# Performance work log

Hardware: AMD Instinct MI355X
Metric: run time of the kernel (lower is better)

The kernel has to match this reference:

```python
import jax, jax.numpy as jnp
import numpy as np

NUM_HEADS = 16


def setup_inputs() -> dict:
    key = jax.random.key(0)
    k1, k2, k3, k4 = jax.random.split(key, 4)
    B, N, C = 4, 2048, 1024
    x = jax.random.normal(k1, (B, N, C), dtype=jnp.float32)
    # xavier-uniform-ish scaling for stable softmax
    Wqkv = jax.random.normal(k2, (C, 3 * C), dtype=jnp.float32) * (2.0 / (C + 3 * C)) ** 0.5
    Wproj = jax.random.normal(k3, (C, C), dtype=jnp.float32) * (1.0 / C) ** 0.5
    bproj = jnp.zeros((C,), dtype=jnp.float32)
    mask = jax.random.randint(k4, (B, N), 0, 2, dtype=jnp.int32)  # >0 means masked
    return {"x": x, "Wqkv": Wqkv, "Wproj": Wproj, "bproj": bproj, "mask": mask}


def reference(x, Wqkv, Wproj, bproj, mask):
    B, N, C = x.shape
    H = NUM_HEADS
    Dh = C // H
    scale = Dh ** -0.5
    qkv = x @ Wqkv                                   # [B, N, 3C]
    qkv = qkv.reshape(B, N, 3, H, Dh).transpose(2, 0, 3, 1, 4)  # [3, B, H, N, Dh]
    q, k, v = qkv[0], qkv[1], qkv[2]
    att = jnp.einsum('bhqd,bhkd->bhqk', q, k) * scale  # [B, H, N, N]
    att = jnp.where(mask[:, None, None, :] > 0, jnp.float32(-10000000.0), att)
    att = jax.nn.softmax(att, axis=-1)
    out = jnp.einsum('bhqk,bhkd->bhqd', att, v)      # [B, H, N, Dh]
    out = out.transpose(0, 2, 1, 3).reshape(B, N, C)
    return out @ Wproj + bproj
```

## Files before the change

### kernel.cpp

```cpp
#include <hip/hip_runtime.h>
#include <hip/hip_bf16.h>
#include <cstdint>

typedef __bf16 bf16x8 __attribute__((ext_vector_type(8)));
typedef float f32x4 __attribute__((ext_vector_type(4)));
typedef uint4 __attribute__((may_alias)) uint4a;
typedef uint2 __attribute__((may_alias)) uint2a;

typedef __attribute__((address_space(3))) unsigned int   lds_u32;
typedef __attribute__((address_space(1))) const unsigned int gbl_u32;

#define BATCH 4
#define SEQ   2048
#define CDIM  1024
#define NH    16
#define HD    64

#define C1SCALE 0.18033688011112042f

__device__ __forceinline__ unsigned short f2bf(float f) {
    uint32_t u = __builtin_bit_cast(uint32_t, f);
    u += 0x7fffu + ((u >> 16) & 1u);
    return (unsigned short)(u >> 16);
}

#if __has_builtin(__builtin_amdgcn_cvt_pk_bf16_f32)
typedef __bf16 bf16x2 __attribute__((ext_vector_type(2)));
__device__ __forceinline__ uint32_t pk2bf(float a, float b) {
    bf16x2 v = __builtin_amdgcn_cvt_pk_bf16_f32(a, b);
    return __builtin_bit_cast(uint32_t, v);
}
#else
__device__ __forceinline__ uint32_t pk2bf(float a, float b) {
    return (uint32_t)f2bf(a) | ((uint32_t)f2bf(b) << 16);
}
#endif

__device__ __forceinline__ void g2l16(const unsigned short* g, unsigned short* l) {
    __builtin_amdgcn_global_load_lds((gbl_u32*)g, (lds_u32*)l, 16, 0, 0);
}

#define NB_CVT   8192
#define NB_TQKV  768
#define NB_TPROJ 256
#define NB_PREP  (NB_CVT + NB_TQKV + NB_TPROJ + 4)

__global__ __launch_bounds__(256)
void prep_kernel(const float* __restrict__ x,
                 const float* __restrict__ Wqkv,
                 const float* __restrict__ Wproj,
                 const int* __restrict__ mask,
                 unsigned short* __restrict__ xb,
                 unsigned short* __restrict__ Wqkvt,
                 unsigned short* __restrict__ Wprojt,
                 int* __restrict__ ridx, int* __restrict__ cnt) {
    __shared__ float tile[64][65];
    __shared__ int s[256];
    int bid = blockIdx.x, tid = threadIdx.x;

    if (bid < NB_CVT) {
        int i = (bid * 256 + tid) * 4;
        float4 v = *(const float4*)(x + i);
        uint2 o;
        o.x = pk2bf(v.x, v.y);
        o.y = pk2bf(v.z, v.w);
        *(uint2*)(xb + i) = o;
        return;
    }
    if (bid < NB_CVT + NB_TQKV + NB_TPROJ) {
        const float* in;
        unsigned short* out;
        int Cc, bx;
        if (bid < NB_CVT + NB_TQKV) {
            bx = bid - NB_CVT; in = Wqkv; out = Wqkvt; Cc = 3072;
        } else {
            bx = bid - NB_CVT - NB_TQKV; in = Wproj; out = Wprojt; Cc = 1024;
        }
        int nbx = Cc >> 6;
        int c0 = (bx % nbx) * 64, r0 = (bx / nbx) * 64;
        int tx = tid & 63, ty = tid >> 6;
        #pragma unroll
        for (int i = 0; i < 64; i += 4)
            tile[ty + i][tx] = in[(size_t)(r0 + ty + i) * Cc + c0 + tx];
        __syncthreads();
        #pragma unroll
        for (int i = 0; i < 64; i += 4)
            out[(size_t)(c0 + ty + i) * 1024 + r0 + tx] = f2bf(tile[tx][ty + i]);
        return;
    }
    int b = bid - (NB_CVT + NB_TQKV + NB_TPROJ);
    int keep[8], lc = 0;
    #pragma unroll
    for (int u = 0; u < 8; ++u) {
        keep[u] = (mask[b * SEQ + tid * 8 + u] > 0) ? 0 : 1;
        lc += keep[u];
    }
    s[tid] = lc;
    __syncthreads();
    for (int d = 1; d < 256; d <<= 1) {
        int w = (tid >= d) ? s[tid - d] : 0;
        __syncthreads();
        s[tid] += w;
        __syncthreads();
    }
    int pos = s[tid] - lc;
    #pragma unroll
    for (int u = 0; u < 8; ++u) {
        if (keep[u]) ridx[b * SEQ + pos++] = tid * 8 + u;
    }
    int total = s[255];
    for (int i = total + tid; i < SEQ; i += 256)
        ridx[b * SEQ + i] = 0;
    if (tid == 255) cnt[b] = total;
}

#define BK 64

__global__ __launch_bounds__(256, 2)
void gemm_qkv2_kernel(const unsigned short* __restrict__ A,
                      const unsigned short* __restrict__ Bt,
                      const int* __restrict__ ridx,
                      const int* __restrict__ cnt,
                      unsigned short* __restrict__ Q,
                      unsigned short* __restrict__ Kc,
                      unsigned short* __restrict__ Vct) {
    __shared__ __align__(16) unsigned short sA[128 * 64];
    __shared__ __align__(16) unsigned short sB[128 * 64];
    const int Kdim = 1024;
    int tid = threadIdx.x;
    int wave = tid >> 6, lane = tid & 63;
    int wm = (wave >> 1) * 64, wn = (wave & 1) * 64;
    int l15 = lane & 15, quad = lane >> 4;
    int lr = lane >> 3, lc8 = ((lane & 7) ^ lr) * 8;

    const bool qpath = (blockIdx.y < 8);
    int m0, n0, b = 0, kn = 0;
    const unsigned short* aPtr[4];

    if (qpath) {
        m0 = blockIdx.x * 128;
        n0 = blockIdx.y * 128;
        #pragma unroll
        for (int it = 0; it < 4; ++it) {
            int gr = (wave * 4 + it) * 8 + lr;
            aPtr[it] = A + (size_t)(m0 + gr) * Kdim + lc8;
        }
    } else {
        b  = blockIdx.x >> 4;
        m0 = (blockIdx.x & 15) * 128;
        kn = cnt[b];
        if (m0 >= kn) return;
        n0 = 1024 + (blockIdx.y - 8) * 128;
        #pragma unroll
        for (int it = 0; it < 4; ++it) {
            int gr = (wave * 4 + it) * 8 + lr;
            int rid = ridx[b * SEQ + m0 + gr];
            aPtr[it] = A + (size_t)(b * SEQ + rid) * Kdim + lc8;
        }
    }

    f32x4 acc[4][4] = {};

    for (int k0 = 0; k0 < Kdim; k0 += BK) {
        #pragma unroll
        for (int it = 0; it < 4; ++it) {
            int c = wave * 4 + it;
            int gr = c * 8 + lr;
            g2l16(aPtr[it] + k0, &sA[c * 512]);
            g2l16(Bt + (size_t)(n0 + gr) * Kdim + k0 + lc8, &sB[c * 512]);
        }
        __syncthreads();
        #pragma unroll
        for (int kk = 0; kk < BK; kk += 32) {
            bf16x8 af[4], bfr[4];
            #pragma unroll
            for (int i = 0; i < 4; ++i) {
                int r = wm + i * 16 + l15;
                int q = ((kk >> 3) + quad) ^ (r & 7);
                af[i] = __builtin_bit_cast(bf16x8, *(const uint4a*)(&sA[r * 64 + q * 8]));
            }
            #pragma unroll
            for (int j = 0; j < 4; ++j) {
                int r = wn + j * 16 + l15;
                int q = ((kk >> 3) + quad) ^ (r & 7);
                bfr[j] = __builtin_bit_cast(bf16x8, *(const uint4a*)(&sB[r * 64 + q * 8]));
            }
            #pragma unroll
            for (int i = 0; i < 4; ++i)
                #pragma unroll
                for (int j = 0; j < 4; ++j)
                    acc[i][j] = __builtin_amdgcn_mfma_f32_16x16x32_bf16(af[i], bfr[j], acc[i][j], 0, 0, 0);
        }
        __syncthreads();
    }

    if (qpath) {
        #pragma unroll
        for (int i = 0; i < 4; ++i) {
            #pragma unroll
            for (int j = 0; j < 4; ++j) {
                int col = n0 + wn + j * 16 + l15;
                int h = col >> 6;
                int d = col & 63;
                int row0 = m0 + wm + i * 16 + quad * 4;
                int bb = row0 >> 11, n = row0 & 2047;
                size_t bh = (size_t)(bb * NH + h);
                uint32_t p01 = pk2bf(acc[i][j][0] * C1SCALE, acc[i][j][1] * C1SCALE);
                uint32_t p23 = pk2bf(acc[i][j][2] * C1SCALE, acc[i][j][3] * C1SCALE);
                size_t base = (bh * SEQ + n) * HD + d;
                Q[base]          = (unsigned short)p01;
                Q[base + HD]     = (unsigned short)(p01 >> 16);
                Q[base + 2 * HD] = (unsigned short)p23;
                Q[base + 3 * HD] = (unsigned short)(p23 >> 16);
            }
        }
    } else {
        #pragma unroll
        for (int i = 0; i < 4; ++i) {
            #pragma unroll
            for (int j = 0; j < 4; ++j) {
                int c2 = (n0 - 1024) + wn + j * 16 + l15;
                int three = c2 >> 10;
                int h = (c2 >> 6) & 15;
                int d = c2 & 63;
                int pf0 = m0 + wm + i * 16 + quad * 4;
                size_t bh = (size_t)(b * NH + h);
                if (three == 0) {
                    #pragma unroll
                    for (int r = 0; r < 4; ++r) {
                        int pf = pf0 + r;
                        if (pf < kn) Kc[(bh * SEQ + pf) * HD + d] = f2bf(acc[i][j][r]);
                    }
                } else {
                    #pragma unroll
                    for (int r = 0; r < 4; ++r) {
                        int pf = pf0 + r;
                        if (pf < kn) Vct[(bh * HD + d) * SEQ + pf] = f2bf(acc[i][j][r]);
                    }
                }
            }
        }
    }
}

__global__ __launch_bounds__(256, 2)
void gemm_proj_kernel(const unsigned short* __restrict__ A,
                      const unsigned short* __restrict__ Bt,
                      const float* __restrict__ bias,
                      float* __restrict__ Out) {
    __shared__ __align__(16) unsigned short sA[128 * 64];
    __shared__ __align__(16) unsigned short sB[128 * 64];
    const int Kdim = 1024;
    int m0 = blockIdx.x * 128;
    int n0 = blockIdx.y * 128;
    int tid = threadIdx.x;
    int wave = tid >> 6, lane = tid & 63;
    int wm = (wave >> 1) * 64, wn = (wave & 1) * 64;
    int l15 = lane & 15, quad = lane >> 4;
    int lr = lane >> 3, lc8 = ((lane & 7) ^ lr) * 8;

    f32x4 acc[4][4] = {};

    for (int k0 = 0; k0 < Kdim; k0 += BK) {
        #pragma unroll
        for (int it = 0; it < 4; ++it) {
            int c = wave * 4 + it;
            int gr = c * 8 + lr;
            g2l16(A  + (size_t)(m0 + gr) * Kdim + k0 + lc8, &sA[c * 512]);
            g2l16(Bt + (size_t)(n0 + gr) * Kdim + k0 + lc8, &sB[c * 512]);
        }
        __syncthreads();
        #pragma unroll
        for (int kk = 0; kk < BK; kk += 32) {
            bf16x8 af[4], bfr[4];
            #pragma unroll
            for (int i = 0; i < 4; ++i) {
                int r = wm + i * 16 + l15;
                int q = ((kk >> 3) + quad) ^ (r & 7);
                af[i] = __builtin_bit_cast(bf16x8, *(const uint4a*)(&sA[r * 64 + q * 8]));
            }
            #pragma unroll
            for (int j = 0; j < 4; ++j) {
                int r = wn + j * 16 + l15;
                int q = ((kk >> 3) + quad) ^ (r & 7);
                bfr[j] = __builtin_bit_cast(bf16x8, *(const uint4a*)(&sB[r * 64 + q * 8]));
            }
            #pragma unroll
            for (int i = 0; i < 4; ++i)
                #pragma unroll
                for (int j = 0; j < 4; ++j)
                    acc[i][j] = __builtin_amdgcn_mfma_f32_16x16x32_bf16(af[i], bfr[j], acc[i][j], 0, 0, 0);
        }
        __syncthreads();
    }

    #pragma unroll
    for (int i = 0; i < 4; ++i) {
        #pragma unroll
        for (int j = 0; j < 4; ++j) {
            int col = n0 + wn + j * 16 + l15;
            float bv = bias[col];
            #pragma unroll
            for (int r = 0; r < 4; ++r) {
                int row = m0 + wm + i * 16 + quad * 4 + r;
                Out[(size_t)row * CDIM + col] = acc[i][j][r] + bv;
            }
        }
    }
}

#define SPD 72

__global__ __launch_bounds__(256, 4)
void flash_attn_kernel(const unsigned short* __restrict__ Q,
                       const unsigned short* __restrict__ Kg,
                       const unsigned short* __restrict__ Vt,
                       const int* __restrict__ cnt,
                       unsigned short* __restrict__ O) {
    int bh = blockIdx.x;
    int q0 = blockIdx.y * 128;
    int b = bh >> 4, h = bh & 15;
    int tid = threadIdx.x;
    int wave = tid >> 6, lane = tid & 63;
    int l15 = lane & 15, quad = lane >> 4;
    int lr = lane >> 3, lc8 = ((lane & 7) ^ lr) * 8;

    const int kn = cnt[b];

    const size_t head_off = (size_t)bh * SEQ * HD;
    const unsigned short* Qh = Q + head_off;
    const unsigned short* Kh = Kg + head_off;
    const unsigned short* Vh = Vt + head_off;

    __shared__ __align__(16) unsigned short sK [64 * 64];
    __shared__ __align__(16) unsigned short sVt[64 * 64];
    __shared__ __align__(16) unsigned short sP [4][32 * SPD];

    bf16x8 qf[2][2];
    #pragma unroll
    for (int mt = 0; mt < 2; ++mt) {
        const unsigned short* qp = Qh + (size_t)(q0 + wave * 32 + mt * 16 + l15) * HD + quad * 8;
        qf[mt][0] = __builtin_bit_cast(bf16x8, *(const uint4a*)(qp));
        qf[mt][1] = __builtin_bit_cast(bf16x8, *(const uint4a*)(qp + 32));
    }

    bf16x8 ones;
    {
        uint4 ov;
        ov.x = ov.y = ov.z = ov.w = 0x3F803F80u;
        ones = __builtin_bit_cast(bf16x8, ov);
    }

    f32x4 oacc[2][4] = {};
    f32x4 oextra[2] = {};

    for (int k0 = 0; k0 < kn; k0 += 64) {
        #pragma unroll
        for (int it = 0; it < 2; ++it) {
            int c = wave * 2 + it;
            int gr = c * 8 + lr;
            g2l16(Kh + (size_t)(k0 + gr) * HD + lc8, &sK[c * 512]);
            g2l16(Vh + (size_t)gr * SEQ + k0 + lc8, &sVt[c * 512]);
        }
        __syncthreads();

        bool tail = (k0 + 64 > kn);

        f32x4 s[2][4] = {};
        #pragma unroll
        for (int j = 0; j < 4; ++j) {
            int r = j * 16 + l15, sw = r & 7;
            uint4 v0 = *(const uint4a*)(&sK[r * 64 + ((quad ^ sw) * 8)]);
            uint4 v1 = *(const uint4a*)(&sK[r * 64 + (((4 + quad) ^ sw) * 8)]);
            bf16x8 k0f = __builtin_bit_cast(bf16x8, v0);
            bf16x8 k1f = __builtin_bit_cast(bf16x8, v1);
            __builtin_amdgcn_s_setprio(1);
            s[0][j] = __builtin_amdgcn_mfma_f32_16x16x32_bf16(k0f, qf[0][0], s[0][j], 0, 0, 0);
            s[0][j] = __builtin_amdgcn_mfma_f32_16x16x32_bf16(k1f, qf[0][1], s[0][j], 0, 0, 0);
            s[1][j] = __builtin_amdgcn_mfma_f32_16x16x32_bf16(k0f, qf[1][0], s[1][j], 0, 0, 0);
            s[1][j] = __builtin_amdgcn_mfma_f32_16x16x32_bf16(k1f, qf[1][1], s[1][j], 0, 0, 0);
            __builtin_amdgcn_s_setprio(0);
        }

        unsigned short* sp = &sP[wave][0];
        #pragma unroll
        for (int mt = 0; mt < 2; ++mt) {
            int row = mt * 16 + l15;
            #pragma unroll
            for (int j = 0; j < 4; ++j) {
                if (tail) {
                    int kb = k0 + j * 16 + quad * 4;
                    #pragma unroll
                    for (int r = 0; r < 4; ++r)
                        s[mt][j][r] = __builtin_amdgcn_exp2f(s[mt][j][r] + ((kb + r < kn) ? 0.f : -1e30f));
                } else {
                    #pragma unroll
                    for (int r = 0; r < 4; ++r)
                        s[mt][j][r] = __builtin_amdgcn_exp2f(s[mt][j][r]);
                }
                uint2 wv;
                wv.x = pk2bf(s[mt][j][0], s[mt][j][1]);
                wv.y = pk2bf(s[mt][j][2], s[mt][j][3]);
                *(uint2a*)(&sp[row * SPD + j * 16 + quad * 4]) = wv;
            }
        }

        #pragma unroll
        for (int kc = 0; kc < 2; ++kc) {
            uint4 a0 = *(const uint4a*)(&sp[(l15)      * SPD + kc * 32 + quad * 8]);
            uint4 a1 = *(const uint4a*)(&sp[(16 + l15) * SPD + kc * 32 + quad * 8]);
            bf16x8 af0 = __builtin_bit_cast(bf16x8, a0);
            bf16x8 af1 = __builtin_bit_cast(bf16x8, a1);
            __builtin_amdgcn_s_setprio(1);
            #pragma unroll
            for (int jd = 0; jd < 4; ++jd) {
                int r = jd * 16 + l15;
                int q = ((kc * 4 + quad) ^ (r & 7)) * 8;
                uint4 bv = *(const uint4a*)(&sVt[r * 64 + q]);
                bf16x8 vf = __builtin_bit_cast(bf16x8, bv);
                oacc[0][jd] = __builtin_amdgcn_mfma_f32_16x16x32_bf16(af0, vf, oacc[0][jd], 0, 0, 0);
                oacc[1][jd] = __builtin_amdgcn_mfma_f32_16x16x32_bf16(af1, vf, oacc[1][jd], 0, 0, 0);
            }
            oextra[0] = __builtin_amdgcn_mfma_f32_16x16x32_bf16(af0, ones, oextra[0], 0, 0, 0);
            oextra[1] = __builtin_amdgcn_mfma_f32_16x16x32_bf16(af1, ones, oextra[1], 0, 0, 0);
            __builtin_amdgcn_s_setprio(0);
        }
        __syncthreads();
    }

    #pragma unroll
    for (int mt = 0; mt < 2; ++mt) {
        float rl[4];
        #pragma unroll
        for (int r = 0; r < 4; ++r) rl[r] = __builtin_amdgcn_rcpf(oextra[mt][r]);
        #pragma unroll
        for (int jd = 0; jd < 4; ++jd) {
            int d = jd * 16 + l15;
            size_t base = ((size_t)(b * SEQ + q0 + wave * 32 + mt * 16 + quad * 4)) * CDIM + h * HD + d;
            uint32_t p01 = pk2bf(oacc[mt][jd][0] * rl[0], oacc[mt][jd][1] * rl[1]);
            uint32_t p23 = pk2bf(oacc[mt][jd][2] * rl[2], oacc[mt][jd][3] * rl[3]);
            O[base]            = (unsigned short)p01;
            O[base + CDIM]     = (unsigned short)(p01 >> 16);
            O[base + 2 * CDIM] = (unsigned short)p23;
            O[base + 3 * CDIM] = (unsigned short)(p23 >> 16);
        }
    }
}

extern "C" void kernel_launch(void* const* d_in, const int* in_sizes, int n_in,
                              void* d_out, int out_size, void* d_ws, size_t ws_size,
                              hipStream_t stream) {
    const float* x     = (const float*)d_in[0];
    const float* Wqkv  = (const float*)d_in[1];
    const float* Wproj = (const float*)d_in[2];
    const float* bproj = (const float*)d_in[3];
    const int*   mask  = (const int*)d_in[4];
    float* out = (float*)d_out;

    char* ws = (char*)d_ws;
    unsigned short* xb     = (unsigned short*)(ws);
    unsigned short* Wqkvt  = (unsigned short*)(ws + (16u << 20));
    unsigned short* Wprojt = (unsigned short*)(ws + (22u << 20));
    unsigned short* Qb     = (unsigned short*)(ws + (24u << 20));
    unsigned short* Kb     = (unsigned short*)(ws + (40u << 20));
    unsigned short* Vtb    = (unsigned short*)(ws + (56u << 20));
    int*            ridx   = (int*)(ws + (72u << 20));
    int*            cntb   = (int*)(ws + (72u << 20) + (32u << 10));

    prep_kernel<<<dim3(NB_PREP), dim3(256), 0, stream>>>(x, Wqkv, Wproj, mask,
                                                         xb, Wqkvt, Wprojt, ridx, cntb);
    gemm_qkv2_kernel<<<dim3(64, 24), dim3(256), 0, stream>>>(xb, Wqkvt, ridx, cntb, Qb, Kb, Vtb);
    flash_attn_kernel<<<dim3(64, 16), dim3(256), 0, stream>>>(Qb, Kb, Vtb, cntb, xb);
    gemm_proj_kernel<<<dim3(64, 8), dim3(256), 0, stream>>>(xb, Wprojt, bproj, out);
}
```

Measured before the change: 226.9 us.

## Fuse all four stages into one cooperative persistent kernel with grid syncs

Turns the prep, QKV GEMM, flash attention and projection kernels into device functions and runs them in one cooperative kernel of 1024 blocks, with grid.sync between stages and grid-stride loops over virtual tiles. The aim is to remove the launch gaps and tails between the four kernels. The cost is that every stage now runs at the fused kernel's launch bounds and shared-memory size, so the GEMMs lose their dedicated occupancy of 2 and may get a different register allocation. Each grid-wide barrier adds latency, and the original launches remain as a fallback if the cooperative launch fails.

After: 636.6 us. 181% more time.

```diff
diff --git a/kernel.cpp b/kernel.cpp
--- a/kernel.cpp
+++ b/kernel.cpp
@@ -1,6 +1,9 @@
 #include <hip/hip_runtime.h>
 #include <hip/hip_bf16.h>
+#include <hip/hip_cooperative_groups.h>
 #include <cstdint>
+
+namespace cg = cooperative_groups;
 
 typedef __bf16 bf16x8 __attribute__((ext_vector_type(8)));
 typedef float f32x4 __attribute__((ext_vector_type(4)));
@@ -44,19 +47,20 @@
 #define NB_TQKV  768
 #define NB_TPROJ 256
 #define NB_PREP  (NB_CVT + NB_TQKV + NB_TPROJ + 4)
-
-__global__ __launch_bounds__(256)
-void prep_kernel(const float* __restrict__ x,
-                 const float* __restrict__ Wqkv,
-                 const float* __restrict__ Wproj,
-                 const int* __restrict__ mask,
-                 unsigned short* __restrict__ xb,
-                 unsigned short* __restrict__ Wqkvt,
-                 unsigned short* __restrict__ Wprojt,
-                 int* __restrict__ ridx, int* __restrict__ cnt) {
-    __shared__ float tile[64][65];
-    __shared__ int s[256];
-    int bid = blockIdx.x, tid = threadIdx.x;
+#define PREP_SMEM 17664
+
+__device__ __forceinline__ void prep_body(
+        int bid, int tid, unsigned char* smem,
+        const float* __restrict__ x,
+        const float* __restrict__ Wqkv,
+        const float* __restrict__ Wproj,
+        const int* __restrict__ mask,
+        unsigned short* __restrict__ xb,
+        unsigned short* __restrict__ Wqkvt,
+        unsigned short* __restrict__ Wprojt,
+        int* __restrict__ ridx, int* __restrict__ cnt) {
+    float (*tile)[65] = (float(*)[65])smem;
+    int* s = (int*)(smem + 64 * 65 * 4);
 
     if (bid < NB_CVT) {
         int i = (bid * 256 + tid) * 4;
@@ -86,6 +90,7 @@
         #pragma unroll
         for (int i = 0; i < 64; i += 4)
             out[(size_t)(c0 + ty + i) * 1024 + r0 + tx] = f2bf(tile[tx][ty + i]);
+        __syncthreads();
         return;
     }
     int b = bid - (NB_CVT + NB_TQKV + NB_TPROJ);
@@ -112,45 +117,47 @@
     for (int i = total + tid; i < SEQ; i += 256)
         ridx[b * SEQ + i] = 0;
     if (tid == 255) cnt[b] = total;
+    __syncthreads();
 }
 
 #define BK 64
-
-__global__ __launch_bounds__(256, 2)
-void gemm_qkv2_kernel(const unsigned short* __restrict__ A,
-                      const unsigned short* __restrict__ Bt,
-                      const int* __restrict__ ridx,
-                      const int* __restrict__ cnt,
-                      unsigned short* __restrict__ Q,
-                      unsigned short* __restrict__ Kc,
-                      unsigned short* __restrict__ Vct) {
-    __shared__ __align__(16) unsigned short sA[128 * 64];
-    __shared__ __align__(16) unsigned short sB[128 * 64];
+#define GEMM_SMEM 32768
+
+__device__ __forceinline__ void qkv2_body(
+        int vx, int vy, int tid, unsigned char* smem,
+        const unsigned short* __restrict__ A,
+        const unsigned short* __restrict__ Bt,
+        const int* __restrict__ ridx,
+        const int* __restrict__ cnt,
+        unsigned short* __restrict__ Q,
+        unsigned short* __restrict__ Kc,
+        unsigned short* __restrict__ Vct) {
+    unsigned short* sA = (unsigned short*)smem;
+    unsigned short* sB = sA + 128 * 64;
     const int Kdim = 1024;
-    int tid = threadIdx.x;
     int wave = tid >> 6, lane = tid & 63;
     int wm = (wave >> 1) * 64, wn = (wave & 1) * 64;
     int l15 = lane & 15, quad = lane >> 4;
     int lr = lane >> 3, lc8 = ((lane & 7) ^ lr) * 8;
 
-    const bool qpath = (blockIdx.y < 8);
+    const bool qpath = (vy < 8);
     int m0, n0, b = 0, kn = 0;
     const unsigned short* aPtr[4];
 
     if (qpath) {
-        m0 = blockIdx.x * 128;
-        n0 = blockIdx.y * 128;
+        m0 = vx * 128;
+        n0 = vy * 128;
         #pragma unroll
         for (int it = 0; it < 4; ++it) {
             int gr = (wave * 4 + it) * 8 + lr;
             aPtr[it] = A + (size_t)(m0 + gr) * Kdim + lc8;
         }
     } else {
-        b  = blockIdx.x >> 4;
-        m0 = (blockIdx.x & 15) * 128;
+        b  = vx >> 4;
+        m0 = (vx & 15) * 128;
         kn = cnt[b];
         if (m0 >= kn) return;
-        n0 = 1024 + (blockIdx.y - 8) * 128;
+        n0 = 1024 + (vy - 8) * 128;
         #pragma unroll
         for (int it = 0; it < 4; ++it) {
             int gr = (wave * 4 + it) * 8 + lr;
@@ -243,17 +250,17 @@
     }
 }
 
-__global__ __launch_bounds__(256, 2)
-void gemm_proj_kernel(const unsigned short* __restrict__ A,
-                      const unsigned short* __restrict__ Bt,
-                      const float* __restrict__ bias,
-                      float* __restrict__ Out) {
-    __shared__ __align__(16) unsigned short sA[128 * 64];
-    __shared__ __align__(16) unsigned short sB[128 * 64];
+__device__ __forceinline__ void proj_body(
+        int vx, int vy, int tid, unsigned char* smem,
+        const unsigned short* __restrict__ A,
+        const unsigned short* __restrict__ Bt,
+        const float* __restrict__ bias,
+        float* __restrict__ Out) {
+    unsigned short* sA = (unsigned short*)smem;
+    unsigned short* sB = sA + 128 * 64;
     const int Kdim = 1024;
-    int m0 = blockIdx.x * 128;
-    int n0 = blockIdx.y * 128;
-    int tid = threadIdx.x;
+    int m0 = vx * 128;
+    int n0 = vy * 128;
     int wave = tid >> 6, lane = tid & 63;
     int wm = (wave >> 1) * 64, wn = (wave & 1) * 64;
     int l15 = lane & 15, quad = lane >> 4;
@@ -310,17 +317,17 @@
 }
 
 #define SPD 72
-
-__global__ __launch_bounds__(256, 4)
-void flash_attn_kernel(const unsigned short* __restrict__ Q,
-                       const unsigned short* __restrict__ Kg,
-                       const unsigned short* __restrict__ Vt,
-                       const int* __restrict__ cnt,
-                       unsigned short* __restrict__ O) {
-    int bh = blockIdx.x;
-    int q0 = blockIdx.y * 128;
+#define FLASH_SMEM 34816
+
+__device__ __forceinline__ void flash_body(
+        int bh, int qy, int tid, unsigned char* smem,
+        const unsigned short* __restrict__ Q,
+        const unsigned short* __restrict__ Kg,
+        const unsigned short* __restrict__ Vt,
+        const int* __restrict__ cnt,
+        unsigned short* __restrict__ O) {
+    int q0 = qy * 128;
     int b = bh >> 4, h = bh & 15;
-    int tid = threadIdx.x;
     int wave = tid >> 6, lane = tid & 63;
     int l15 = lane & 15, quad = lane >> 4;
     int lr = lane >> 3, lc8 = ((lane & 7) ^ lr) * 8;
@@ -332,9 +339,9 @@
     const unsigned short* Kh = Kg + head_off;
     const unsigned short* Vh = Vt + head_off;
 
-    __shared__ __align__(16) unsigned short sK [64 * 64];
-    __shared__ __align__(16) unsigned short sVt[64 * 64];
-    __shared__ __align__(16) unsigned short sP [4][32 * SPD];
+    unsigned short* sK  = (unsigned short*)smem;
+    unsigned short* sVt = sK + 64 * 64;
+    unsigned short* sP  = sVt + 64 * 64;
 
     bf16x8 qf[2][2];
     #pragma unroll
@@ -382,7 +389,7 @@
             __builtin_amdgcn_s_setprio(0);
         }
 
-        unsigned short* sp = &sP[wave][0];
+        unsigned short* sp = sP + wave * 32 * SPD;
         #pragma unroll
         for (int mt = 0; mt < 2; ++mt) {
             int row = mt * 16 + l15;
@@ -447,6 +454,69 @@
     }
 }
 
+#define NBLK 1024
+
+__global__ __launch_bounds__(256, 4)
+void mega_kernel(const float* x, const float* Wqkv, const float* Wproj,
+                 const float* bproj, const int* mask,
+                 unsigned short* xb, unsigned short* Wqkvt, unsigned short* Wprojt,
+                 unsigned short* Qb, unsigned short* Kb, unsigned short* Vtb,
+                 int* ridx, int* cnt, float* out) {
+    cg::grid_group grid = cg::this_grid();
+    __shared__ __align__(16) unsigned char smem[FLASH_SMEM];
+    int bid = blockIdx.x, tid = threadIdx.x;
+
+    for (int vt = bid; vt < NB_PREP; vt += NBLK)
+        prep_body(vt, tid, smem, x, Wqkv, Wproj, mask, xb, Wqkvt, Wprojt, ridx, cnt);
+    grid.sync();
+    for (int vt = bid; vt < 64 * 24; vt += NBLK)
+        qkv2_body(vt & 63, vt >> 6, tid, smem, xb, Wqkvt, ridx, cnt, Qb, Kb, Vtb);
+    grid.sync();
+    for (int vt = bid; vt < 64 * 16; vt += NBLK)
+        flash_body(vt & 63, vt >> 6, tid, smem, Qb, Kb, Vtb, cnt, xb);
+    grid.sync();
+    for (int vt = bid; vt < 64 * 8; vt += NBLK)
+        proj_body(vt & 63, vt >> 6, tid, smem, xb, Wprojt, bproj, out);
+}
+
+__global__ __launch_bounds__(256)
+void prep_kernel(const float* __restrict__ x, const float* __restrict__ Wqkv,
+                 const float* __restrict__ Wproj, const int* __restrict__ mask,
+                 unsigned short* __restrict__ xb, unsigned short* __restrict__ Wqkvt,
+                 unsigned short* __restrict__ Wprojt,
+                 int* __restrict__ ridx, int* __restrict__ cnt) {
+    __shared__ __align__(16) unsigned char smem[PREP_SMEM];
+    prep_body(blockIdx.x, threadIdx.x, smem, x, Wqkv, Wproj, mask, xb, Wqkvt, Wprojt, ridx, cnt);
+}
+
+__global__ __launch_bounds__(256, 2)
+void gemm_qkv2_kernel(const unsigned short* __restrict__ A,
+                      const unsigned short* __restrict__ Bt,
+                      const int* __restrict__ ridx, const int* __restrict__ cnt,
+                      unsigned short* __restrict__ Q, unsigned short* __restrict__ Kc,
+                      unsigned short* __restrict__ Vct) {
+    __shared__ __align__(16) unsigned char smem[GEMM_SMEM];
+    qkv2_body(blockIdx.x, blockIdx.y, threadIdx.x, smem, A, Bt, ridx, cnt, Q, Kc, Vct);
+}
+
+__global__ __launch_bounds__(256, 2)
+void gemm_proj_kernel(const unsigned short* __restrict__ A,
+                      const unsigned short* __restrict__ Bt,
+                      const float* __restrict__ bias, float* __restrict__ Out) {
+    __shared__ __align__(16) unsigned char smem[GEMM_SMEM];
+    proj_body(blockIdx.x, blockIdx.y, threadIdx.x, smem, A, Bt, bias, Out);
+}
+
+__global__ __launch_bounds__(256, 4)
+void flash_attn_kernel(const unsigned short* __restrict__ Q,
+                       const unsigned short* __restrict__ Kg,
+                       const unsigned short* __restrict__ Vt,
+                       const int* __restrict__ cnt,
+                       unsigned short* __restrict__ O) {
+    __shared__ __align__(16) unsigned char smem[FLASH_SMEM];
+    flash_body(blockIdx.x, blockIdx.y, threadIdx.x, smem, Q, Kg, Vt, cnt, O);
+}
+
 extern "C" void kernel_launch(void* const* d_in, const int* in_sizes, int n_in,
                               void* d_out, int out_size, void* d_ws, size_t ws_size,
                               hipStream_t stream) {
@@ -467,9 +537,18 @@
     int*            ridx   = (int*)(ws + (72u << 20));
     int*            cntb   = (int*)(ws + (72u << 20) + (32u << 10));
 
-    prep_kernel<<<dim3(NB_PREP), dim3(256), 0, stream>>>(x, Wqkv, Wproj, mask,
-                                                         xb, Wqkvt, Wprojt, ridx, cntb);
-    gemm_qkv2_kernel<<<dim3(64, 24), dim3(256), 0, stream>>>(xb, Wqkvt, ridx, cntb, Qb, Kb, Vtb);
-    flash_attn_kernel<<<dim3(64, 16), dim3(256), 0, stream>>>(Qb, Kb, Vtb, cntb, xb);
-    gemm_proj_kernel<<<dim3(64, 8), dim3(256), 0, stream>>>(xb, Wprojt, bproj, out);
-}
+    void* args[14] = { (void*)&x, (void*)&Wqkv, (void*)&Wproj, (void*)&bproj,
+                       (void*)&mask, (void*)&xb, (void*)&Wqkvt, (void*)&Wprojt,
+                       (void*)&Qb, (void*)&Kb, (void*)&Vtb,
+                       (void*)&ridx, (void*)&cntb, (void*)&out };
+    hipError_t err = hipLaunchCooperativeKernel((const void*)mega_kernel,
+                                                dim3(NBLK), dim3(256),
+                                                args, 0u, stream);
+    if (err != hipSuccess) {
+        prep_kernel<<<dim3(NB_PREP), dim3(256), 0, stream>>>(x, Wqkv, Wproj, mask,
+                                                             xb, Wqkvt, Wprojt, ridx, cntb);
+        gemm_qkv2_kernel<<<dim3(64, 24), dim3(256), 0, stream>>>(xb, Wqkvt, ridx, cntb, Qb, Kb, Vtb);
+        flash_attn_kernel<<<dim3(64, 16), dim3(256), 0, stream>>>(Qb, Kb, Vtb, cntb, xb);
+        gemm_proj_kernel<<<dim3(64, 8), dim3(256), 0, stream>>>(xb, Wprojt, bproj, out);
+    }
+}
```
